# Kernel tuning notes

Hardware: AMD Instinct MI355X
Metric: run time of the kernel (lower is better)

## Reference

```python
import jax, jax.numpy as jnp
import numpy as np

IMAGE_WEIGHT = 0.0736196319
EXAM_WEIGHTS = np.array([0.0736196319, 0.09202453988, 0.1042944785, 0.1042944785,
                         0.1877300613, 0.06257668712, 0.06257668712, 0.2346625767,
                         0.0782208589], dtype=np.float32)


def setup_inputs() -> dict:
    key = jax.random.key(0)
    k1, k2, k3 = jax.random.split(key, 3)
    B, L, C = 128, 8192, 10
    # probabilities / soft labels in (0,1); keep away from exact 0/1 so log() is finite
    pred = jax.random.uniform(k1, (B, L, C), dtype=jnp.float32) * 0.98 + 0.01
    label = jax.random.uniform(k2, (B, L, C), dtype=jnp.float32) * 0.98 + 0.01
    seq_lens = jax.random.randint(k3, (B,), 1, L + 1, dtype=jnp.int32)
    return {"pred": pred, "label": label, "seq_lens": seq_lens}


def reference(pred, label, seq_lens):
    B, L, C = pred.shape
    w = jnp.asarray(EXAM_WEIGHTS, dtype=pred.dtype)          # [9]
    lens = seq_lens.astype(pred.dtype)                        # [B]
    mask = (jnp.arange(L)[None, :] < seq_lens[:, None]).astype(pred.dtype)  # [B, L]

    # ---- exam-level loss: BCE between per-exam masked means, weighted per channel ----
    pm = jnp.einsum('blc,bl->bc', pred[..., 1:], mask) / lens[:, None]   # [B, 9]
    ym = jnp.einsum('blc,bl->bc', label[..., 1:], mask) / lens[:, None]  # [B, 9]
    exam_bce = -(ym * jnp.log(pm) + (1.0 - ym) * jnp.log(1.0 - pm))      # [B, 9]
    exam_loss = jnp.sum(exam_bce * w[None, :])
    total_weights = B * jnp.sum(w)

    # ---- image-level loss: per-element BCE weighted by image_weight * mean(label_0) ----
    p0 = pred[..., 0]   # [B, L]
    y0 = label[..., 0]  # [B, L]
    y0_mean = jnp.sum(y0 * mask, axis=1) / lens                          # [B]
    img_w = IMAGE_WEIGHT * y0_mean                                       # [B]
    img_bce = -(y0 * jnp.log(p0) + (1.0 - y0) * jnp.log(1.0 - p0)) * mask  # [B, L]
    image_loss = jnp.sum(jnp.sum(img_bce, axis=1) * img_w)
    total_weights = total_weights + jnp.sum(img_w * lens)

    return (exam_loss + image_loss) / total_weights
```

## Files before the change

### kernel.cpp

```cpp
#include <hip/hip_runtime.h>


#define L_DIM 8192
#define B_DIM 128
#define C_DIM 10
#define SPLIT 8

#define IMAGE_WEIGHT 0.0736196319f

__device__ __constant__ float EXAM_W[9] = {
    0.0736196319f, 0.09202453988f, 0.1042944785f, 0.1042944785f,
    0.1877300613f, 0.06257668712f, 0.06257668712f, 0.2346625767f,
    0.0782208589f};

__global__ __launch_bounds__(256) void rsna_partial_kernel(
    const float* __restrict__ pred, const float* __restrict__ label,
    const int* __restrict__ seq_lens, float* __restrict__ row_acc) {
  const int b = blockIdx.x;
  const int s = blockIdx.y;
  const int len = seq_lens[b];
  const int chunk = (len + SPLIT - 1) / SPLIT;
  const int start = s * chunk;
  const int end = min(start + chunk, len);

  float sp[9], sl[9];
#pragma unroll
  for (int c = 0; c < 9; ++c) {
    sp[c] = 0.0f;
    sl[c] = 0.0f;
  }
  float sy0 = 0.0f;
  float sbce = 0.0f;

  for (int l = start + (int)threadIdx.x; l < end; l += 256) {
    const size_t base = ((size_t)b * L_DIM + (size_t)l) * C_DIM;
    const float2* p2 = reinterpret_cast<const float2*>(pred + base);
    const float2* y2 = reinterpret_cast<const float2*>(label + base);
    float p[10], y[10];
#pragma unroll
    for (int i = 0; i < 5; ++i) {
      float2 pv = p2[i];
      float2 yv = y2[i];
      p[2 * i] = pv.x;
      p[2 * i + 1] = pv.y;
      y[2 * i] = yv.x;
      y[2 * i + 1] = yv.y;
    }
#pragma unroll
    for (int c = 0; c < 9; ++c) {
      sp[c] += p[c + 1];
      sl[c] += y[c + 1];
    }
    sy0 += y[0];
    sbce += -(y[0] * __logf(p[0]) + (1.0f - y[0]) * __logf(1.0f - p[0]));
  }

  float vals[20];
#pragma unroll
  for (int c = 0; c < 9; ++c) {
    vals[c] = sp[c];
    vals[9 + c] = sl[c];
  }
  vals[18] = sy0;
  vals[19] = sbce;

#pragma unroll
  for (int i = 0; i < 20; ++i) {
    float v = vals[i];
#pragma unroll
    for (int off = 32; off > 0; off >>= 1) v += __shfl_down(v, off, 64);
    vals[i] = v;
  }

  __shared__ float lds[4][20];
  const int wave = threadIdx.x >> 6;
  const int lane = threadIdx.x & 63;
  if (lane == 0) {
#pragma unroll
    for (int i = 0; i < 20; ++i) lds[wave][i] = vals[i];
  }
  __syncthreads();
  if (threadIdx.x < 20) {
    const float v = lds[0][threadIdx.x] + lds[1][threadIdx.x] +
                    lds[2][threadIdx.x] + lds[3][threadIdx.x];
    atomicAdd(&row_acc[b * 20 + (int)threadIdx.x], v);
  }
}

__global__ __launch_bounds__(128) void rsna_final_kernel(
    const float* __restrict__ row_acc, const int* __restrict__ seq_lens,
    float* __restrict__ out) {
  const int b = threadIdx.x;
  const float* r = row_acc + b * 20;
  const float len = (float)seq_lens[b];
  const float inv_len = 1.0f / len;

  float exam = 0.0f;
#pragma unroll
  for (int c = 0; c < 9; ++c) {
    const float pm = r[c] * inv_len;
    const float ym = r[9 + c] * inv_len;
    const float bce = -(ym * __logf(pm) + (1.0f - ym) * __logf(1.0f - pm));
    exam += EXAM_W[c] * bce;
  }
  const float sy0 = r[18];
  const float sbce = r[19];
  const float img_w = IMAGE_WEIGHT * sy0 * inv_len;
  float numer = exam + sbce * img_w;
  float wext = IMAGE_WEIGHT * sy0;

#pragma unroll
  for (int off = 32; off > 0; off >>= 1) {
    numer += __shfl_down(numer, off, 64);
    wext += __shfl_down(wext, off, 64);
  }

  __shared__ float lds[4];
  if ((threadIdx.x & 63) == 0) {
    const int wave = threadIdx.x >> 6;
    lds[wave * 2] = numer;
    lds[wave * 2 + 1] = wext;
  }
  __syncthreads();
  if (threadIdx.x == 0) {
    float wsum = 0.0f;
#pragma unroll
    for (int c = 0; c < 9; ++c) wsum += EXAM_W[c];
    const float n = lds[0] + lds[2];
    const float w = lds[1] + lds[3];
    out[0] = n / ((float)B_DIM * wsum + w);
  }
}

extern "C" void kernel_launch(void* const* d_in, const int* in_sizes, int n_in,
                              void* d_out, int out_size, void* d_ws,
                              size_t ws_size, hipStream_t stream) {
  const float* pred = (const float*)d_in[0];
  const float* label = (const float*)d_in[1];
  const int* seq_lens = (const int*)d_in[2];
  float* row_acc = (float*)d_ws;

  hipMemsetAsync(d_ws, 0, B_DIM * 20 * sizeof(float), stream);

  dim3 grid(B_DIM, SPLIT);
  rsna_partial_kernel<<<grid, 256, 0, stream>>>(pred, label, seq_lens, row_acc);
  rsna_final_kernel<<<1, 128, 0, stream>>>(row_acc, seq_lens, (float*)d_out);
}
```

Measured before the change: 111.4 us.

## Load row pairs with float4 and replace atomics with per-split partial buffers

Rounds each split's chunk to an even length so every thread can process two consecutive rows with five aligned float4 loads instead of ten float2 loads, which is meant to make global memory access wider. A single-thread tail handles an odd final row. The atomicAdd accumulation and the memset are replaced by per-(batch, split) partial stores, which the final kernel sums. This removes the memset launch and the atomics at the cost of a slightly larger reduction in the final kernel.

```diff
diff --git a/kernel.cpp b/kernel.cpp
--- a/kernel.cpp
+++ b/kernel.cpp
@@ -19,9 +19,11 @@
   const int b = blockIdx.x;
   const int s = blockIdx.y;
   const int len = seq_lens[b];
-  const int chunk = (len + SPLIT - 1) / SPLIT;
+  int chunk = (len + SPLIT - 1) / SPLIT;
+  chunk = (chunk + 1) & ~1;
   const int start = s * chunk;
   const int end = min(start + chunk, len);
+  const int n = end - start;
 
   float sp[9], sl[9];
 #pragma unroll
@@ -32,27 +34,62 @@
   float sy0 = 0.0f;
   float sbce = 0.0f;
 
-  for (int l = start + (int)threadIdx.x; l < end; l += 256) {
-    const size_t base = ((size_t)b * L_DIM + (size_t)l) * C_DIM;
-    const float2* p2 = reinterpret_cast<const float2*>(pred + base);
-    const float2* y2 = reinterpret_cast<const float2*>(label + base);
-    float p[10], y[10];
+  if (n > 0) {
+    const int npair = n >> 1;
+    const size_t base = ((size_t)b * L_DIM + (size_t)start) * C_DIM;
+    const float4* p4base = reinterpret_cast<const float4*>(pred + base);
+    const float4* y4base = reinterpret_cast<const float4*>(label + base);
+
+    for (int t = (int)threadIdx.x; t < npair; t += 256) {
+      const float4* p4 = p4base + (size_t)t * 5;
+      const float4* y4 = y4base + (size_t)t * 5;
+      float p[20], y[20];
 #pragma unroll
-    for (int i = 0; i < 5; ++i) {
-      float2 pv = p2[i];
-      float2 yv = y2[i];
-      p[2 * i] = pv.x;
-      p[2 * i + 1] = pv.y;
-      y[2 * i] = yv.x;
-      y[2 * i + 1] = yv.y;
+      for (int j = 0; j < 5; ++j) {
+        const float4 pv = p4[j];
+        const float4 yv = y4[j];
+        p[4 * j + 0] = pv.x;
+        p[4 * j + 1] = pv.y;
+        p[4 * j + 2] = pv.z;
+        p[4 * j + 3] = pv.w;
+        y[4 * j + 0] = yv.x;
+        y[4 * j + 1] = yv.y;
+        y[4 * j + 2] = yv.z;
+        y[4 * j + 3] = yv.w;
+      }
+#pragma unroll
+      for (int c = 0; c < 9; ++c) {
+        sp[c] += p[c + 1] + p[c + 11];
+        sl[c] += y[c + 1] + y[c + 11];
+      }
+      sy0 += y[0] + y[10];
+      sbce += -(y[0] * __logf(p[0]) + (1.0f - y[0]) * __logf(1.0f - p[0]));
+      sbce += -(y[10] * __logf(p[10]) + (1.0f - y[10]) * __logf(1.0f - p[10]));
     }
+
+    if ((n & 1) && threadIdx.x == 0) {
+      const int l = end - 1;
+      const size_t tbase = ((size_t)b * L_DIM + (size_t)l) * C_DIM;
+      const float2* p2 = reinterpret_cast<const float2*>(pred + tbase);
+      const float2* y2 = reinterpret_cast<const float2*>(label + tbase);
+      float p[10], y[10];
 #pragma unroll
-    for (int c = 0; c < 9; ++c) {
-      sp[c] += p[c + 1];
-      sl[c] += y[c + 1];
+      for (int i = 0; i < 5; ++i) {
+        const float2 pv = p2[i];
+        const float2 yv = y2[i];
+        p[2 * i] = pv.x;
+        p[2 * i + 1] = pv.y;
+        y[2 * i] = yv.x;
+        y[2 * i + 1] = yv.y;
+      }
+#pragma unroll
+      for (int c = 0; c < 9; ++c) {
+        sp[c] += p[c + 1];
+        sl[c] += y[c + 1];
+      }
+      sy0 += y[0];
+      sbce += -(y[0] * __logf(p[0]) + (1.0f - y[0]) * __logf(1.0f - p[0]));
     }
-    sy0 += y[0];
-    sbce += -(y[0] * __logf(p[0]) + (1.0f - y[0]) * __logf(1.0f - p[0]));
   }
 
   float vals[20];
@@ -83,7 +120,7 @@
   if (threadIdx.x < 20) {
     const float v = lds[0][threadIdx.x] + lds[1][threadIdx.x] +
                     lds[2][threadIdx.x] + lds[3][threadIdx.x];
-    atomicAdd(&row_acc[b * 20 + (int)threadIdx.x], v);
+    row_acc[(b * SPLIT + s) * 20 + (int)threadIdx.x] = v;
   }
 }
 
@@ -91,7 +128,23 @@
     const float* __restrict__ row_acc, const int* __restrict__ seq_lens,
     float* __restrict__ out) {
   const int b = threadIdx.x;
-  const float* r = row_acc + b * 20;
+
+  float r[20];
+#pragma unroll
+  for (int i = 0; i < 20; ++i) r[i] = 0.0f;
+  for (int s = 0; s < SPLIT; ++s) {
+    const float4* seg =
+        reinterpret_cast<const float4*>(row_acc + ((size_t)b * SPLIT + s) * 20);
+#pragma unroll
+    for (int j = 0; j < 5; ++j) {
+      const float4 v = seg[j];
+      r[4 * j + 0] += v.x;
+      r[4 * j + 1] += v.y;
+      r[4 * j + 2] += v.z;
+      r[4 * j + 3] += v.w;
+    }
+  }
+
   const float len = (float)seq_lens[b];
   const float inv_len = 1.0f / len;
 
@@ -140,8 +193,6 @@
   const int* seq_lens = (const int*)d_in[2];
   float* row_acc = (float*)d_ws;
 
-  hipMemsetAsync(d_ws, 0, B_DIM * 20 * sizeof(float), stream);
-
   dim3 grid(B_DIM, SPLIT);
   rsna_partial_kernel<<<grid, 256, 0, stream>>>(pred, label, seq_lens, row_acc);
   rsna_final_kernel<<<1, 128, 0, stream>>>(row_acc, seq_lens, (float*)d_out);
```

Result: no change. 111.9 us, median of 2 (+0.4%).
